# Kernel optimization log

Measured on AMD Instinct MI355X. Metric: run time of the kernel, lower is better.

The kernel has to match this reference:

```python
import jax, jax.numpy as jnp
import numpy as np
from jax import lax

B, U, D = 16, 2048, 512


def setup_inputs() -> dict:
    key = jax.random.key(0)
    ks = jax.random.split(key, 6)
    xs = jax.random.normal(ks[0], (B, U, D), dtype=jnp.float32)
    xlens = jax.random.randint(ks[1], (B,), U // 2, U + 1).astype(jnp.int32)
    ylens = jax.random.randint(ks[2], (B,), 128, 257).astype(jnp.int32)
    # Conv1d(D, D, kernel_size=3, padding=1): weight [O, I, K], bias [O]
    conv_w = jax.random.normal(ks[3], (D, D, 3), dtype=jnp.float32) * (1.0 / np.sqrt(3 * D))
    conv_b = jnp.zeros((D,), dtype=jnp.float32)
    # Linear(D, 1)
    lin_w = jax.random.normal(ks[4], (1, D), dtype=jnp.float32) * (1.0 / np.sqrt(D))
    lin_b = jnp.zeros((1,), dtype=jnp.float32)
    return {"xs": xs, "xlens": xlens, "ylens": ylens,
            "conv_w": conv_w, "conv_b": conv_b, "lin_w": lin_w, "lin_b": lin_b}


def _forward(xs, xlens, ylens, conv_w, conv_b, lin_w, lin_b, u_max):
    # alpha gate: conv1d -> relu -> linear -> sigmoid
    h = lax.conv_general_dilated(xs.transpose(0, 2, 1), conv_w, (1,), ((1, 1),),
                                 dimension_numbers=("NCH", "OIH", "NCH"))
    h = jax.nn.relu(h + conv_b[None, :, None])          # [B, D, U]
    alpha = jax.nn.sigmoid(jnp.einsum("bdu,od->bu", h, lin_w) + lin_b[0])  # [B, U]
    # zero padded positions (positions >= xlen)
    pos = jnp.arange(U)[None, :]
    alpha = jnp.where(pos >= xlens[:, None], 0.0, alpha)
    sum_alpha = alpha.sum(-1)                            # [B]
    beta = sum_alpha / ylens.astype(sum_alpha.dtype) - 1e-4  # [B]

    def step(carry, inp):
        prev_alpha, prev_state = carry                   # [B], [B, D]
        cur_alpha, cur_state = inp                       # [B], [B, D]
        new_alpha = prev_alpha + cur_alpha
        fired = new_alpha >= beta                        # [B]
        left = (beta - prev_alpha)[:, None]
        right = (new_alpha - beta)[:, None]
        integ = prev_state + left * cur_state            # integrated state at fire
        next_alpha = jnp.where(fired, right[:, 0], new_alpha)
        next_state = jnp.where(fired[:, None], right * cur_state, integ)
        next_fired = jnp.where(fired[:, None], integ, jnp.zeros_like(integ))
        return (next_alpha, next_state), next_fired

    init = (jnp.zeros((B,), xs.dtype), jnp.zeros((B, D), xs.dtype))
    _, fired_seq = lax.scan(step, init, (alpha.T, xs.transpose(1, 0, 2)))
    fired_state = fired_seq.transpose(1, 0, 2)           # [B, U, D]

    # stable-move fired frames to the front of each batch row
    marks = jnp.abs(fired_state).sum(-1) != 0.0          # [B, U] bool
    order = jnp.argsort(~marks, axis=1, stable=True)     # fired (False-key) first
    cif_output = jnp.take_along_axis(fired_state, order[:, :, None], axis=1)
    h_cif = cif_output[:, :u_max, :]
    return h_cif, sum_alpha


def reference(xs, xlens, ylens, conv_w, conv_b, lin_w, lin_b):
    u_max = int(jnp.max(ylens))
    return _forward(xs, xlens, ylens, conv_w, conv_b, lin_w, lin_b, u_max)
```

## Files before the change

### kernel.cpp

```cpp
#include <hip/hip_runtime.h>
#include <cstddef>
#include <cstdint>

#define Bb 16
#define Uu 2048
#define Dd 512
#define BU (Bb*Uu)

typedef short bf16x8 __attribute__((ext_vector_type(8)));
typedef float f32x4 __attribute__((ext_vector_type(4)));

#define A_PLANE 2080
#define A_SPLIT 8320
#define A_BYTES 16640
#define B_SLICE 16384
#define B_BASE  16640
#define STEP_BYTES 65536
#define SMEM_BYTES (B_BASE + 2*B_SLICE)

#define WAITVM(N) asm volatile("s_waitcnt vmcnt(" #N ")" ::: "memory")
#define WAITLGKM0 asm volatile("s_waitcnt lgkmcnt(0)" ::: "memory")

__device__ __forceinline__ unsigned short f2bf(float x){
  unsigned int u = __float_as_uint(x);
  u += 0x7fff + ((u >> 16) & 1);
  return (unsigned short)(u >> 16);
}
__device__ __forceinline__ float bf2f(unsigned short b){
  return __uint_as_float(((unsigned int)b) << 16);
}

union U16x8 { unsigned short s[8]; uint4 v; };

__device__ __forceinline__ void split2(float x, unsigned short& h, unsigned short& m){
  h = f2bf(x);
  float r1 = x - bf2f(h);
  m = f2bf(r1);
}

__global__ __launch_bounds__(256) void pack_b_kernel(const float* __restrict__ conv_w,
                                                     char* __restrict__ Bpack){
  int idx = blockIdx.x * 256 + threadIdx.x;
  int n = idx >> 6, cg = idx & 63;
  int chunk = cg >> 2, lg = cg & 3, c0 = cg << 3;
  const float* src = conv_w + (size_t)n * (Dd * 3) + (size_t)c0 * 3;
  float w[24];
  #pragma unroll
  for (int j = 0; j < 24; ++j) w[j] = src[j];
  int cs = n >> 7, cc = n & 127, cgrp = cc >> 4, li = cc & 15;
  char* base = Bpack + (size_t)cs * B_SLICE + cgrp * 2048 + lg * 256 + li * 16;
  #pragma unroll
  for (int tap = 0; tap < 3; ++tap){
    U16x8 H, M;
    #pragma unroll
    for (int j = 0; j < 8; ++j) split2(w[j * 3 + tap], H.s[j], M.s[j]);
    char* dst = base + (size_t)(chunk * 3 + tap) * STEP_BYTES;
    *(uint4*)dst = H.v;
    *(uint4*)(dst + 1024) = M.v;
  }
}

__device__ __forceinline__ void stage_A_direct(char* abuf, const float* __restrict__ xsb,
                                               int u0, int c0, int tid){
  #pragma unroll
  for (int it = 0; it < 3; ++it){
    if (it < 2 || tid < 8){
      int t = (it < 2) ? (tid + it * 256) : (512 + tid);
      int r = t >> 2, lgw = t & 3;
      int uu = u0 - 1 + r;
      float x[8];
      if (uu >= 0 && uu < Uu){
        const float* p = xsb + (size_t)uu * Dd + c0 + lgw * 8;
        float4 a = *(const float4*)p;
        float4 b = *(const float4*)(p + 4);
        x[0]=a.x; x[1]=a.y; x[2]=a.z; x[3]=a.w; x[4]=b.x; x[5]=b.y; x[6]=b.z; x[7]=b.w;
      } else {
        #pragma unroll
        for (int j = 0; j < 8; ++j) x[j] = 0.f;
      }
      U16x8 H, M;
      #pragma unroll
      for (int j = 0; j < 8; ++j) split2(x[j], H.s[j], M.s[j]);
      char* dst = abuf + lgw * A_PLANE + r * 16;
      *(uint4*)(dst)           = H.v;
      *(uint4*)(dst + A_SPLIT) = M.v;
    }
  }
}

__device__ __forceinline__ void gll16(const char* g, char* l){
  __builtin_amdgcn_global_load_lds(
      (const __attribute__((address_space(1))) unsigned int*)g,
      (__attribute__((address_space(3))) unsigned int*)l, 16, 0, 0);
}

__device__ __forceinline__ void stage_slice(char* ldsB, const char* __restrict__ src,
                                            int lane, int wv){
  const char* g = src + wv * 1024 + lane * 16;
  char* l = ldsB + wv * 1024;
  gll16(g, l);
  gll16(g + 4096,  l + 4096);
  gll16(g + 8192,  l + 8192);
  gll16(g + 12288, l + 12288);
}

__device__ __forceinline__ bf16x8 ldfrag(const char* p){
  return __builtin_bit_cast(bf16x8, *(const uint4*)p);
}

__global__ __launch_bounds__(256, 3) void conv_mfma_full_kernel(
    const float* __restrict__ xs, const char* __restrict__ Bpack,
    const float* __restrict__ conv_b, const float* __restrict__ lin_w,
    const int* __restrict__ xlens,
    float* __restrict__ partial)
{
  __shared__ __align__(16) char smem[SMEM_BYTES];
  const int tid = threadIdx.x;
  const int lane = tid & 63, wv = tid >> 6;
  const int wm = wv >> 1;
  const int wn = wv & 1;
  const int ut = blockIdx.x >> 6;
  const int cs = (blockIdx.x >> 4) & 3;
  const int b  = blockIdx.x & 15;
  const int u0 = ut * 128;
  if (u0 >= xlens[b]) return;
  const float* xsb = xs + (size_t)b * Uu * Dd;
  const int li = lane & 15, lg = lane >> 4;

  f32x4 acc[4][4];
  #pragma unroll
  for (int m = 0; m < 4; ++m)
    #pragma unroll
    for (int n = 0; n < 4; ++n){
      f32x4 z = {0.f, 0.f, 0.f, 0.f};
      acc[m][n] = z;
    }

  stage_A_direct(smem, xsb, u0, 0, tid);
  stage_slice(smem + B_BASE, Bpack + (size_t)cs * B_SLICE, lane, wv);
  __syncthreads();

  for (int chunk = 0; chunk < 16; ++chunk){
    const bool more = (chunk < 15);
    char* aC = smem;

    bf16x8 a[4][2];
    #pragma unroll
    for (int m = 0; m < 4; ++m){
      const char* ar = aC + lg * A_PLANE + (size_t)(wm * 64 + m * 16 + li) * 16;
      a[m][0] = ldfrag(ar);
      a[m][1] = ldfrag(ar + A_SPLIT);
    }

    #pragma unroll
    for (int tap = 0; tap < 3; ++tap){
      const int p = chunk * 3 + tap;
      const int bbuf = p & 1;
      const bool apf_now = (tap == 2) && more;

      float4 pa0, pa1, pb0, pb1, pe0, pe1;
      int rA = 0, cgA = 0, rE = 0, lgE = 0;
      bool aval = true, eval_ = true;
      if (apf_now){
        const float4 z4 = make_float4(0.f,0.f,0.f,0.f);
        int c0n = (chunk + 1) * 32;
        rA = tid >> 2; cgA = tid & 3;
        int uuA = u0 - 1 + rA;
        aval = (uuA >= 0);
        int uuAc = aval ? uuA : 0;
        const float* pp = xsb + (size_t)uuAc * Dd + c0n + cgA * 8;
        pa0 = *(const float4*)pp;
        pa1 = *(const float4*)(pp + 4);
        if (!aval){ pa0 = z4; pa1 = z4; }
        const float* pq = xsb + (size_t)(u0 + 63 + rA) * Dd + c0n + cgA * 8;
        pb0 = *(const float4*)pq;
        pb1 = *(const float4*)(pq + 4);
        int q = wv * 2 + lane;
        rE = 128 + (q >> 2); lgE = q & 3;
        int uuE = u0 - 1 + rE;
        eval_ = (uuE < Uu);
        int uuEc = eval_ ? uuE : (Uu - 1);
        pe0 = z4; pe1 = z4;
        if (lane < 2){
          const float* pr = xsb + (size_t)uuEc * Dd + c0n + lgE * 8;
          pe0 = *(const float4*)pr;
          pe1 = *(const float4*)(pr + 4);
        }
        if (!eval_){ pe0 = z4; pe1 = z4; }
        __builtin_amdgcn_sched_barrier(0);
      }

      if (p < 47)
        stage_slice(smem + B_BASE + (bbuf ^ 1) * B_SLICE,
                    Bpack + (size_t)(p + 1) * STEP_BYTES + (size_t)cs * B_SLICE, lane, wv);

      if (p == 47)       { WAITVM(0); }
      else if (apf_now)  { WAITVM(10); }
      else               { WAITVM(4); }
      __builtin_amdgcn_sched_barrier(0);

      __builtin_amdgcn_s_setprio(1);
      const char* bbase = smem + B_BASE + bbuf * B_SLICE;
      #pragma unroll
      for (int n = 0; n < 4; ++n){
        const char* br = bbase + (size_t)(wn * 4 + n) * 2048 + lg * 256 + li * 16;
        bf16x8 bh = ldfrag(br);
        bf16x8 bm = ldfrag(br + 1024);
        #pragma unroll
        for (int m = 0; m < 4; ++m) acc[m][n] = __builtin_amdgcn_mfma_f32_16x16x32_bf16(a[m][0], bh, acc[m][n], 0, 0, 0);
        #pragma unroll
        for (int m = 0; m < 4; ++m) acc[m][n] = __builtin_amdgcn_mfma_f32_16x16x32_bf16(a[m][1], bh, acc[m][n], 0, 0, 0);
        #pragma unroll
        for (int m = 0; m < 4; ++m) acc[m][n] = __builtin_amdgcn_mfma_f32_16x16x32_bf16(a[m][0], bm, acc[m][n], 0, 0, 0);
        #pragma unroll
        for (int m = 0; m < 4; ++m) acc[m][n] = __builtin_amdgcn_mfma_f32_16x16x32_bf16(a[m][1], bm, acc[m][n], 0, 0, 0);
      }
      __builtin_amdgcn_s_setprio(0);

      if (tap < 2){
        #pragma unroll
        for (int m = 0; m < 4; ++m){
          const char* ar = aC + lg * A_PLANE + (size_t)(wm * 64 + m * 16 + li + tap + 1) * 16;
          a[m][0] = ldfrag(ar);
          a[m][1] = ldfrag(ar + A_SPLIT);
        }
      }

      if (apf_now){
        WAITVM(4);
        __builtin_amdgcn_sched_barrier(0);
        __builtin_amdgcn_s_barrier();
        U16x8 H, M;
        float x[8];
        x[0]=pa0.x; x[1]=pa0.y; x[2]=pa0.z; x[3]=pa0.w;
        x[4]=pa1.x; x[5]=pa1.y; x[6]=pa1.z; x[7]=pa1.w;
        #pragma unroll
        for (int jj = 0; jj < 8; ++jj) split2(x[jj], H.s[jj], M.s[jj]);
        char* dA = aC + cgA * A_PLANE + rA * 16;
        *(uint4*)(dA)           = H.v;
        *(uint4*)(dA + A_SPLIT) = M.v;
        x[0]=pb0.x; x[1]=pb0.y; x[2]=pb0.z; x[3]=pb0.w;
        x[4]=pb1.x; x[5]=pb1.y; x[6]=pb1.z; x[7]=pb1.w;
        #pragma unroll
        for (int jj = 0; jj < 8; ++jj) split2(x[jj], H.s[jj], M.s[jj]);
        char* dB = aC + cgA * A_PLANE + (64 + rA) * 16;
        *(uint4*)(dB)           = H.v;
        *(uint4*)(dB + A_SPLIT) = M.v;
        if (lane < 2){
          float y[8];
          y[0]=pe0.x; y[1]=pe0.y; y[2]=pe0.z; y[3]=pe0.w;
          y[4]=pe1.x; y[5]=pe1.y; y[6]=pe1.z; y[7]=pe1.w;
          #pragma unroll
          for (int jj = 0; jj < 8; ++jj) split2(y[jj], H.s[jj], M.s[jj]);
          char* dE = aC + lgE * A_PLANE + rE * 16;
          *(uint4*)(dE)           = H.v;
          *(uint4*)(dE + A_SPLIT) = M.v;
        }
        WAITLGKM0;
        __builtin_amdgcn_sched_barrier(0);
      }
      __builtin_amdgcn_s_barrier();
    }
  }

  __syncthreads();
  float* pbuf = (float*)smem;
  #pragma unroll
  for (int m = 0; m < 4; ++m){
    float s0 = 0.f, s1 = 0.f, s2 = 0.f, s3 = 0.f;
    #pragma unroll
    for (int n = 0; n < 4; ++n){
      int col = cs * 128 + wn * 64 + n * 16 + li;
      float cb = conv_b[col], lw = lin_w[col];
      f32x4 v = acc[m][n];
      float h;
      h = v[0] + cb; h = h > 0.f ? h : 0.f; s0 += h * lw;
      h = v[1] + cb; h = h > 0.f ? h : 0.f; s1 += h * lw;
      h = v[2] + cb; h = h > 0.f ? h : 0.f; s2 += h * lw;
      h = v[3] + cb; h = h > 0.f ? h : 0.f; s3 += h * lw;
    }
    #pragma unroll
    for (int msk = 1; msk < 16; msk <<= 1){
      s0 += __shfl_xor(s0, msk); s1 += __shfl_xor(s1, msk);
      s2 += __shfl_xor(s2, msk); s3 += __shfl_xor(s3, msk);
    }
    if (li == 0){
      int fr = wm * 64 + m * 16 + lg * 4;
      pbuf[(fr + 0) * 2 + wn] = s0;
      pbuf[(fr + 1) * 2 + wn] = s1;
      pbuf[(fr + 2) * 2 + wn] = s2;
      pbuf[(fr + 3) * 2 + wn] = s3;
    }
  }
  __syncthreads();
  if (tid < 128){
    float pv = pbuf[tid * 2] + pbuf[tid * 2 + 1];
    partial[(size_t)cs * BU + (size_t)b * Uu + u0 + tid] = pv;
  }
}

__global__ __launch_bounds__(64) void scan_kernel(
    const float* __restrict__ partial, const float* __restrict__ lin_b,
    const int* __restrict__ xlens, const int* __restrict__ ylens,
    float* __restrict__ wA, float* __restrict__ wB,
    int* __restrict__ fire_pos, int* __restrict__ nf,
    float* __restrict__ out_sum)
{
  __shared__ float salpha[Uu];
  int b = blockIdx.x;
  int lane = threadIdx.x;
  int xl = xlens[b];
  int xce = (xl + 63) & ~63;
  float lb = lin_b[0];

  float sum = 0.f;
  for (int u0 = 0; u0 < xce; u0 += 64){
    int u = u0 + lane;
    size_t ix = (size_t)b * Uu + u;
    float v = lb + partial[ix] + partial[BU + ix] + partial[2 * BU + ix] + partial[3 * BU + ix];
    float a = 1.f / (1.f + expf(-v));
    if (u >= xl) a = 0.f;
    salpha[u] = a;
    sum += a;
  }
  #pragma unroll
  for (int m = 1; m < 64; m <<= 1) sum += __shfl_xor(sum, m);
  float sa = sum;
  float beta = sa / (float)ylens[b] - 1e-4f;
  if (lane == 0) out_sum[b] = sa;

  float prev = 0.f;
  int cnt = 0;
  for (int u0 = 0; u0 < Uu; u0 += 64) {
    if (u0 >= xl) break;
    float val = salpha[u0 + lane];
    float mywa = 0.f, mywb = 0.f;
    #pragma unroll
    for (int i = 0; i < 64; ++i) {
      float a_cur = __builtin_bit_cast(float,
          __builtin_amdgcn_readlane(__builtin_bit_cast(int, val), i));
      float nw = prev + a_cur;
      float left = beta - prev;
      float right = nw - beta;
      bool fired = nw >= beta;
      if (lane == i) { mywa = left; mywb = right; }
      if (fired) {
        if (lane == 0) fire_pos[(b << 11) + cnt] = u0 + i;
        ++cnt;
      }
      prev = fired ? right : nw;
    }
    wA[(size_t)b * Uu + u0 + lane] = mywa;
    wB[(size_t)b * Uu + u0 + lane] = mywb;
  }
  if (lane == 0) nf[b] = cnt;
}

__global__ __launch_bounds__(512) void gather_kernel(
    const float* __restrict__ xs, const float* __restrict__ wA, const float* __restrict__ wB,
    const int* __restrict__ fire_pos, const int* __restrict__ nf,
    float* __restrict__ out, int umax)
{
  int t = blockIdx.x, b = blockIdx.y;
  int tid = threadIdx.x;
  float* o = out + ((size_t)b * umax + t) * Dd;
  int n = nf[b];
  if (t >= n) { o[tid] = 0.f; return; }
  int start = (t == 0) ? 0 : fire_pos[(b << 11) + t - 1];
  int end = fire_pos[(b << 11) + t];
  const float* xb = xs + (size_t)b * Uu * Dd;
  float acc = 0.f;
  for (int u = start; u <= end; ++u) {
    float w = (t > 0 && u == start) ? wB[(size_t)b * Uu + u] : wA[(size_t)b * Uu + u];
    acc += w * xb[(size_t)u * Dd + tid];
  }
  o[tid] = acc;
}

extern "C" void kernel_launch(void* const* d_in, const int* in_sizes, int n_in,
                              void* d_out, int out_size, void* d_ws, size_t ws_size,
                              hipStream_t stream) {
  const float* xs     = (const float*)d_in[0];
  const int*   xlens  = (const int*)d_in[1];
  const int*   ylens  = (const int*)d_in[2];
  const float* conv_w = (const float*)d_in[3];
  const float* conv_b = (const float*)d_in[4];
  const float* lin_w  = (const float*)d_in[5];
  const float* lin_b  = (const float*)d_in[6];
  float* out = (float*)d_out;
  int umax = (out_size - Bb) / (Bb * Dd);

  char* ws = (char*)d_ws;
  char*  Bpack    = ws;
  float* partial  = (float*)(ws + 48 * (size_t)STEP_BYTES);
  float* wAv      = partial + 4 * BU;
  float* wBv      = wAv + BU;
  int*   fire_pos = (int*)(wBv + BU);
  int*   nf       = (int*)(fire_pos + BU);

  pack_b_kernel<<<(512 * 64) / 256, 256, 0, stream>>>(conv_w, Bpack);
  conv_mfma_full_kernel<<<1024, 256, 0, stream>>>(xs, Bpack, conv_b, lin_w, xlens, partial);
  scan_kernel<<<Bb, 64, 0, stream>>>(partial, lin_b, xlens, ylens, wAv, wBv, fire_pos, nf,
                                     out + (size_t)Bb * umax * Dd);
  if (umax > 0)
    gather_kernel<<<dim3(umax, Bb), 512, 0, stream>>>(xs, wAv, wBv, fire_pos, nf, out, umax);
}
```

Before: 277.9 us.

## Pre-split xs into bf16 hi/lo planes and DMA A tiles into LDS

Measured after the change: 286.8 us. 1.03x slower.

```diff
diff --git a/kernel.cpp b/kernel.cpp
--- a/kernel.cpp
+++ b/kernel.cpp
@@ -18,6 +18,11 @@
 #define STEP_BYTES 65536
 #define SMEM_BYTES (B_BASE + 2*B_SLICE)
 
+#define XSP_PLANE 32896
+#define XSP_CHUNK 263168
+#define XSP_BATCH 4210688
+#define XSP_BYTES (16ull * XSP_BATCH)
+
 #define WAITVM(N) asm volatile("s_waitcnt vmcnt(" #N ")" ::: "memory")
 #define WAITLGKM0 asm volatile("s_waitcnt lgkmcnt(0)" ::: "memory")
 
@@ -57,6 +62,201 @@
     char* dst = base + (size_t)(chunk * 3 + tap) * STEP_BYTES;
     *(uint4*)dst = H.v;
     *(uint4*)(dst + 1024) = M.v;
+  }
+}
+
+__global__ __launch_bounds__(256) void pack_xs_kernel(const float* __restrict__ xs,
+                                                      char* __restrict__ xsp){
+  int b = blockIdx.y;
+  int row = blockIdx.x * 16 + (threadIdx.x >> 4);
+  int chunk = threadIdx.x & 15;
+  if (row >= 2050) return;
+  int u = row - 1;
+  float x[32];
+  if (u >= 0 && u < Uu){
+    const float4* p = (const float4*)(xs + (size_t)b * Uu * Dd + (size_t)u * Dd + chunk * 32);
+    #pragma unroll
+    for (int j = 0; j < 8; ++j){
+      float4 v = p[j];
+      x[j*4]=v.x; x[j*4+1]=v.y; x[j*4+2]=v.z; x[j*4+3]=v.w;
+    }
+  } else {
+    #pragma unroll
+    for (int j = 0; j < 32; ++j) x[j] = 0.f;
+  }
+  char* base = xsp + (size_t)b * XSP_BATCH + (size_t)chunk * XSP_CHUNK + (size_t)row * 16;
+  #pragma unroll
+  for (int lg = 0; lg < 4; ++lg){
+    U16x8 H, M;
+    #pragma unroll
+    for (int j = 0; j < 8; ++j) split2(x[lg*8+j], H.s[j], M.s[j]);
+    *(uint4*)(base + (size_t)lg * XSP_PLANE)       = H.v;
+    *(uint4*)(base + (size_t)(4+lg) * XSP_PLANE)   = M.v;
+  }
+}
+
+__device__ __forceinline__ void gll16(const char* g, char* l){
+  __builtin_amdgcn_global_load_lds(
+      (const __attribute__((address_space(1))) unsigned int*)g,
+      (__attribute__((address_space(3))) unsigned int*)l, 16, 0, 0);
+}
+
+__device__ __forceinline__ void stage_slice(char* ldsB, const char* __restrict__ src,
+                                            int lane, int wv){
+  const char* g = src + wv * 1024 + lane * 16;
+  char* l = ldsB + wv * 1024;
+  gll16(g, l);
+  gll16(g + 4096,  l + 4096);
+  gll16(g + 8192,  l + 8192);
+  gll16(g + 12288, l + 12288);
+}
+
+__device__ __forceinline__ void stage_A_dma(char* ldsA, const char* __restrict__ xspb,
+                                            int chunk, int u0, int lane, int wv){
+  #pragma unroll
+  for (int i = 0; i < 2; ++i){
+    int P = wv * 2 + i;
+    const char* g = xspb + (size_t)chunk * XSP_CHUNK + (size_t)P * XSP_PLANE
+                    + (size_t)u0 * 16 + lane * 16;
+    char* l = ldsA + P * A_PLANE;
+    gll16(g, l);
+    gll16(g + 1024, l + 1024);
+    if (lane < 2) gll16(g + 2048, l + 2048);
+  }
+}
+
+__device__ __forceinline__ bf16x8 ldfrag(const char* p){
+  return __builtin_bit_cast(bf16x8, *(const uint4*)p);
+}
+
+__global__ __launch_bounds__(256, 3) void conv_v15_kernel(
+    const char* __restrict__ xsp, const char* __restrict__ Bpack,
+    const float* __restrict__ conv_b, const float* __restrict__ lin_w,
+    const int* __restrict__ xlens,
+    float* __restrict__ partial)
+{
+  __shared__ __align__(16) char smem[SMEM_BYTES];
+  const int tid = threadIdx.x;
+  const int lane = tid & 63, wv = tid >> 6;
+  const int wm = wv >> 1;
+  const int wn = wv & 1;
+  const int ut = blockIdx.x >> 6;
+  const int cs = (blockIdx.x >> 4) & 3;
+  const int b  = blockIdx.x & 15;
+  const int u0 = ut * 128;
+  if (u0 >= xlens[b]) return;
+  const char* xspb = xsp + (size_t)b * XSP_BATCH;
+  const int li = lane & 15, lg = lane >> 4;
+
+  f32x4 acc[4][4];
+  #pragma unroll
+  for (int m = 0; m < 4; ++m)
+    #pragma unroll
+    for (int n = 0; n < 4; ++n){
+      f32x4 z = {0.f, 0.f, 0.f, 0.f};
+      acc[m][n] = z;
+    }
+
+  stage_A_dma(smem, xspb, 0, u0, lane, wv);
+  stage_slice(smem + B_BASE, Bpack + (size_t)cs * B_SLICE, lane, wv);
+  __syncthreads();
+
+  bf16x8 a[4][2];
+
+  for (int chunk = 0; chunk < 16; ++chunk){
+    const bool more = (chunk < 15);
+    #pragma unroll
+    for (int tap = 0; tap < 3; ++tap){
+      const int p = chunk * 3 + tap;
+      const int bbuf = p & 1;
+
+      if (tap < 2)
+        stage_slice(smem + B_BASE + (bbuf ^ 1) * B_SLICE,
+                    Bpack + (size_t)(p + 1) * STEP_BYTES + (size_t)cs * B_SLICE, lane, wv);
+
+      if (tap < 2) { WAITVM(4); } else { WAITVM(0); }
+      __builtin_amdgcn_sched_barrier(0);
+      __builtin_amdgcn_s_barrier();
+
+      if (tap == 0){
+        #pragma unroll
+        for (int m = 0; m < 4; ++m){
+          const char* ar = smem + lg * A_PLANE + (size_t)(wm * 64 + m * 16 + li) * 16;
+          a[m][0] = ldfrag(ar);
+          a[m][1] = ldfrag(ar + A_SPLIT);
+        }
+      }
+
+      __builtin_amdgcn_s_setprio(1);
+      const char* bbase = smem + B_BASE + bbuf * B_SLICE;
+      #pragma unroll
+      for (int n = 0; n < 4; ++n){
+        const char* br = bbase + (size_t)(wn * 4 + n) * 2048 + lg * 256 + li * 16;
+        bf16x8 bh = ldfrag(br);
+        bf16x8 bm = ldfrag(br + 1024);
+        #pragma unroll
+        for (int m = 0; m < 4; ++m) acc[m][n] = __builtin_amdgcn_mfma_f32_16x16x32_bf16(a[m][0], bh, acc[m][n], 0, 0, 0);
+        #pragma unroll
+        for (int m = 0; m < 4; ++m) acc[m][n] = __builtin_amdgcn_mfma_f32_16x16x32_bf16(a[m][1], bh, acc[m][n], 0, 0, 0);
+        #pragma unroll
+        for (int m = 0; m < 4; ++m) acc[m][n] = __builtin_amdgcn_mfma_f32_16x16x32_bf16(a[m][0], bm, acc[m][n], 0, 0, 0);
+        #pragma unroll
+        for (int m = 0; m < 4; ++m) acc[m][n] = __builtin_amdgcn_mfma_f32_16x16x32_bf16(a[m][1], bm, acc[m][n], 0, 0, 0);
+      }
+      __builtin_amdgcn_s_setprio(0);
+
+      if (tap < 2){
+        #pragma unroll
+        for (int m = 0; m < 4; ++m){
+          const char* ar = smem + lg * A_PLANE + (size_t)(wm * 64 + m * 16 + li + tap + 1) * 16;
+          a[m][0] = ldfrag(ar);
+          a[m][1] = ldfrag(ar + A_SPLIT);
+        }
+      }
+
+      __builtin_amdgcn_s_barrier();
+      if (tap == 2 && more){
+        stage_A_dma(smem, xspb, chunk + 1, u0, lane, wv);
+        stage_slice(smem + B_BASE + (bbuf ^ 1) * B_SLICE,
+                    Bpack + (size_t)(p + 1) * STEP_BYTES + (size_t)cs * B_SLICE,
+                    lane, wv);
+      }
+    }
+  }
+
+  __syncthreads();
+  float* pbuf = (float*)smem;
+  #pragma unroll
+  for (int m = 0; m < 4; ++m){
+    float s0 = 0.f, s1 = 0.f, s2 = 0.f, s3 = 0.f;
+    #pragma unroll
+    for (int n = 0; n < 4; ++n){
+      int col = cs * 128 + wn * 64 + n * 16 + li;
+      float cb = conv_b[col], lw = lin_w[col];
+      f32x4 v = acc[m][n];
+      float h;
+      h = v[0] + cb; h = h > 0.f ? h : 0.f; s0 += h * lw;
+      h = v[1] + cb; h = h > 0.f ? h : 0.f; s1 += h * lw;
+      h = v[2] + cb; h = h > 0.f ? h : 0.f; s2 += h * lw;
+      h = v[3] + cb; h = h > 0.f ? h : 0.f; s3 += h * lw;
+    }
+    #pragma unroll
+    for (int msk = 1; msk < 16; msk <<= 1){
+      s0 += __shfl_xor(s0, msk); s1 += __shfl_xor(s1, msk);
+      s2 += __shfl_xor(s2, msk); s3 += __shfl_xor(s3, msk);
+    }
+    if (li == 0){
+      int fr = wm * 64 + m * 16 + lg * 4;
+      pbuf[(fr + 0) * 2 + wn] = s0;
+      pbuf[(fr + 1) * 2 + wn] = s1;
+      pbuf[(fr + 2) * 2 + wn] = s2;
+      pbuf[(fr + 3) * 2 + wn] = s3;
+    }
+  }
+  __syncthreads();
+  if (tid < 128){
+    float pv = pbuf[tid * 2] + pbuf[tid * 2 + 1];
+    partial[(size_t)cs * BU + (size_t)b * Uu + u0 + tid] = pv;
   }
 }
 
@@ -88,27 +288,7 @@
   }
 }
 
-__device__ __forceinline__ void gll16(const char* g, char* l){
-  __builtin_amdgcn_global_load_lds(
-      (const __attribute__((address_space(1))) unsigned int*)g,
-      (__attribute__((address_space(3))) unsigned int*)l, 16, 0, 0);
-}
-
-__device__ __forceinline__ void stage_slice(char* ldsB, const char* __restrict__ src,
-                                            int lane, int wv){
-  const char* g = src + wv * 1024 + lane * 16;
-  char* l = ldsB + wv * 1024;
-  gll16(g, l);
-  gll16(g + 4096,  l + 4096);
-  gll16(g + 8192,  l + 8192);
-  gll16(g + 12288, l + 12288);
-}
-
-__device__ __forceinline__ bf16x8 ldfrag(const char* p){
-  return __builtin_bit_cast(bf16x8, *(const uint4*)p);
-}
-
-__global__ __launch_bounds__(256, 3) void conv_mfma_full_kernel(
+__global__ __launch_bounds__(256, 3) void conv_r12_kernel(
     const float* __restrict__ xs, const char* __restrict__ Bpack,
     const float* __restrict__ conv_b, const float* __restrict__ lin_w,
     const int* __restrict__ xlens,
@@ -397,9 +577,17 @@
   float* wBv      = wAv + BU;
   int*   fire_pos = (int*)(wBv + BU);
   int*   nf       = (int*)(fire_pos + BU);
+  size_t xsp_off  = 4067328ull;
+  char*  xsp      = ws + xsp_off;
+  size_t need     = xsp_off + XSP_BYTES;
 
   pack_b_kernel<<<(512 * 64) / 256, 256, 0, stream>>>(conv_w, Bpack);
-  conv_mfma_full_kernel<<<1024, 256, 0, stream>>>(xs, Bpack, conv_b, lin_w, xlens, partial);
+  if (ws_size >= need) {
+    pack_xs_kernel<<<dim3(129, 16), 256, 0, stream>>>(xs, xsp);
+    conv_v15_kernel<<<1024, 256, 0, stream>>>(xsp, Bpack, conv_b, lin_w, xlens, partial);
+  } else {
+    conv_r12_kernel<<<1024, 256, 0, stream>>>(xs, Bpack, conv_b, lin_w, xlens, partial);
+  }
   scan_kernel<<<Bb, 64, 0, stream>>>(partial, lin_b, xlens, ylens, wAv, wBv, fire_pos, nf,
                                      out + (size_t)Bb * umax * Dd);
   if (umax > 0)
```
